# Kernel optimization log

Hardware: AMD Instinct MI355X
Metric: run time of the kernel (lower is better)

## Reference

```python
import jax, jax.numpy as jnp
import numpy as np

N, D = 16384, 128

def setup_inputs() -> dict:
    key = jax.random.key(0)
    k1, k2 = jax.random.split(key)
    x = jax.random.normal(k1, (N, D), dtype=jnp.float32)
    adj = jax.random.randint(k2, (N, N), 0, 2, dtype=jnp.int32)
    return {"x": x, "adj": adj}

def reference(x, adj):
    # out[i] = x[i] + sum_{j: adj[i,j]==1} x[j]  ==  (adj + I) @ x
    a = adj.astype(x.dtype)
    return x + jnp.matmul(a, x)  # [N, D]
```

## Files before the change

### kernel.cpp

```cpp
#include <hip/hip_runtime.h>
#include <hip/hip_bf16.h>

#define GN 16384
#define GD 128
#define KSPLIT 4
#define KBLK (GN / KSPLIT)
#define OUT_ELEMS (GN * GD)

typedef __attribute__((ext_vector_type(8))) short short8;
typedef __attribute__((ext_vector_type(4))) float floatx4;
typedef __attribute__((ext_vector_type(4))) int intx4;

static __device__ __forceinline__ unsigned short f32_to_bf16(float f) {
  unsigned u = __builtin_bit_cast(unsigned, f);
  unsigned r = u + 0x7FFFu + ((u >> 16) & 1u);
  return (unsigned short)(r >> 16);
}

__global__ __launch_bounds__(256) void prep_kernel(const float* __restrict__ x,
                                                   unsigned short* __restrict__ xT) {
  __shared__ unsigned short t[GD][66];
  const int tid = threadIdx.x;
  const int j0 = blockIdx.x * 64;
  for (int i = tid; i < 64 * GD; i += 256) {
    int j = i >> 7, d = i & (GD - 1);
    t[d][j] = f32_to_bf16(x[(size_t)(j0 + j) * GD + d]);
  }
  __syncthreads();
  for (int i = tid; i < GD * 32; i += 256) {
    int d = i >> 5, jp = i & 31;
    unsigned lo = t[d][2 * jp], hi = t[d][2 * jp + 1];
    *reinterpret_cast<unsigned*>(xT + (size_t)d * GN + j0 + 2 * jp) = lo | (hi << 16);
  }
}

__global__ __launch_bounds__(64, 2) void gemm_kernel(const int* __restrict__ adj,
                                                     const unsigned short* __restrict__ xT,
                                                     float* __restrict__ partials) {
  const int lane = threadIdx.x;
  const int q = lane >> 4;
  const int m = lane & 15;
  const int wid = blockIdx.x;
  const int rbase = (wid >> 2) * 32;
  const int ks = wid & 3;
  const int kbase = ks * KBLK;

  const int* a0 = adj + (size_t)(rbase + m) * GN + kbase + q * 8;
  const int* a1 = a0 + (size_t)16 * GN;
  const unsigned short* b0 = xT + (size_t)m * GN + kbase + q * 8;

  floatx4 acc[2][8];
#pragma unroll
  for (int t = 0; t < 2; ++t)
#pragma unroll
    for (int c = 0; c < 8; ++c) acc[t][c] = (floatx4){0.f, 0.f, 0.f, 0.f};

  intx4 r0 = __builtin_nontemporal_load((const intx4*)(a0));
  intx4 r1 = __builtin_nontemporal_load((const intx4*)(a0 + 4));
  intx4 r2 = __builtin_nontemporal_load((const intx4*)(a1));
  intx4 r3 = __builtin_nontemporal_load((const intx4*)(a1 + 4));
  short8 bf[8];
#pragma unroll
  for (int c = 0; c < 8; ++c)
    bf[c] = *(const short8*)(b0 + (size_t)c * 16 * GN);

  for (int k = 0; k < KBLK; k += 32) {
    const int kn = (k + 32) & (KBLK - 1);

    intx4 s0 = __builtin_nontemporal_load((const intx4*)(a0 + kn));
    intx4 s1 = __builtin_nontemporal_load((const intx4*)(a0 + kn + 4));
    intx4 s2 = __builtin_nontemporal_load((const intx4*)(a1 + kn));
    intx4 s3 = __builtin_nontemporal_load((const intx4*)(a1 + kn + 4));
    short8 nbf[8];
#pragma unroll
    for (int c = 0; c < 8; ++c)
      nbf[c] = *(const short8*)(b0 + (size_t)c * 16 * GN + kn);

    intx4 p0, p1;
    p0.x = (r0.x | (r0.y << 16)) * 0x3F80;
    p0.y = (r0.z | (r0.w << 16)) * 0x3F80;
    p0.z = (r1.x | (r1.y << 16)) * 0x3F80;
    p0.w = (r1.z | (r1.w << 16)) * 0x3F80;
    p1.x = (r2.x | (r2.y << 16)) * 0x3F80;
    p1.y = (r2.z | (r2.w << 16)) * 0x3F80;
    p1.z = (r3.x | (r3.y << 16)) * 0x3F80;
    p1.w = (r3.z | (r3.w << 16)) * 0x3F80;
    short8 af0 = __builtin_bit_cast(short8, p0);
    short8 af1 = __builtin_bit_cast(short8, p1);

#pragma unroll
    for (int c = 0; c < 8; ++c) {
      acc[0][c] = __builtin_amdgcn_mfma_f32_16x16x32_bf16(af0, bf[c], acc[0][c], 0, 0, 0);
      acc[1][c] = __builtin_amdgcn_mfma_f32_16x16x32_bf16(af1, bf[c], acc[1][c], 0, 0, 0);
    }

    r0 = s0; r1 = s1; r2 = s2; r3 = s3;
#pragma unroll
    for (int c = 0; c < 8; ++c) bf[c] = nbf[c];
  }

  float* pp = partials + (size_t)ks * OUT_ELEMS + (size_t)rbase * GD;
#pragma unroll
  for (int t = 0; t < 2; ++t)
#pragma unroll
    for (int c = 0; c < 8; ++c)
#pragma unroll
      for (int r = 0; r < 4; ++r) {
        int row = t * 16 + q * 4 + r;
        int col = c * 16 + m;
        pp[(size_t)row * GD + col] = acc[t][c][r];
      }
}

__global__ __launch_bounds__(256) void reduce_kernel(const float* __restrict__ x,
                                                     const float* __restrict__ partials,
                                                     float* __restrict__ out) {
  size_t i = ((size_t)blockIdx.x * 256 + threadIdx.x) * 4;
  floatx4 v = *(const floatx4*)(x + i);
  v += *(const floatx4*)(partials + 0 * (size_t)OUT_ELEMS + i);
  v += *(const floatx4*)(partials + 1 * (size_t)OUT_ELEMS + i);
  v += *(const floatx4*)(partials + 2 * (size_t)OUT_ELEMS + i);
  v += *(const floatx4*)(partials + 3 * (size_t)OUT_ELEMS + i);
  *(floatx4*)(out + i) = v;
}

extern "C" void kernel_launch(void* const* d_in, const int* in_sizes, int n_in,
                              void* d_out, int out_size, void* d_ws, size_t ws_size,
                              hipStream_t stream) {
  const float* x = (const float*)d_in[0];
  const int* adj = (const int*)d_in[1];
  float* out = (float*)d_out;
  unsigned short* xT = (unsigned short*)d_ws;
  float* partials = (float*)((char*)d_ws + (size_t)GN * GD * 2);

  prep_kernel<<<GN / 64, 256, 0, stream>>>(x, xT);
  gemm_kernel<<<(GN / 32) * KSPLIT, 64, 0, stream>>>(adj, xT, partials);
  reduce_kernel<<<OUT_ELEMS / 4 / 256, 256, 0, stream>>>(x, partials, out);
}
```

Before: 1.555 ms.

## Share B tiles across four waves via double-buffered LDS with direct global-to-LDS loads

The GEMM kernel moves from single-wave blocks that each read their own copy of the bf16 x^T tile from global memory to 256-thread blocks. In these, four waves share one B tile staged into a double-buffered, XOR-swizzled LDS buffer through global_load_lds. Each wave now covers 16 rows instead of 32, so it holds half the accumulators, which should allow higher occupancy. The intent is to cut redundant global/L2 traffic for B and leave more bandwidth for streaming the int32 adjacency matrix. The cost is a block-wide barrier on every k-step and LDS read overhead.

After: 1.373 ms. -11.8%, faster.

```diff
diff --git a/kernel.cpp b/kernel.cpp
--- a/kernel.cpp
+++ b/kernel.cpp
@@ -5,6 +5,9 @@
 #define GD 128
 #define KSPLIT 4
 #define KBLK (GN / KSPLIT)
+#define BK 64
+#define NPER (KBLK / BK)
+#define BUF_SHORTS (GD * BK)
 #define OUT_ELEMS (GN * GD)
 
 typedef __attribute__((ext_vector_type(8))) short short8;
@@ -34,82 +37,97 @@
   }
 }
 
-__global__ __launch_bounds__(64, 2) void gemm_kernel(const int* __restrict__ adj,
-                                                     const unsigned short* __restrict__ xT,
-                                                     float* __restrict__ partials) {
-  const int lane = threadIdx.x;
+__global__ __launch_bounds__(256, 4) void gemm_kernel(const int* __restrict__ adj,
+                                                      const unsigned short* __restrict__ xT,
+                                                      float* __restrict__ partials) {
+  __shared__ unsigned short bbuf[2][BUF_SHORTS];
+  const int tid = threadIdx.x;
+  const int wave = tid >> 6;
+  const int lane = tid & 63;
   const int q = lane >> 4;
   const int m = lane & 15;
-  const int wid = blockIdx.x;
-  const int rbase = (wid >> 2) * 32;
-  const int ks = wid & 3;
+  const int rbase = blockIdx.x * 64 + wave * 16;
+  const int ks = blockIdx.y;
   const int kbase = ks * KBLK;
 
+  const unsigned short* gptr[4];
+  unsigned short* lptr[4];
+#pragma unroll
+  for (int p = 0; p < 4; ++p) {
+    int s = tid + 256 * p;
+    int n = s >> 3;
+    int gsrc = (s & 7) ^ (n & 7);
+    gptr[p] = xT + (size_t)n * GN + kbase + gsrc * 8;
+    lptr[p] = &bbuf[0][0] + (size_t)s * 8;
+  }
+
+#define STAGE(bufsel, koff)                                                             \
+  do {                                                                                  \
+    _Pragma("unroll") for (int p = 0; p < 4; ++p) {                                     \
+      __builtin_amdgcn_global_load_lds(                                                 \
+          (const __attribute__((address_space(1))) unsigned int*)(gptr[p] + (koff)),    \
+          (__attribute__((address_space(3))) unsigned int*)(lptr[p] +                   \
+                                                           (bufsel) * BUF_SHORTS),      \
+          16, 0, 0);                                                                    \
+    }                                                                                   \
+  } while (0)
+
   const int* a0 = adj + (size_t)(rbase + m) * GN + kbase + q * 8;
-  const int* a1 = a0 + (size_t)16 * GN;
-  const unsigned short* b0 = xT + (size_t)m * GN + kbase + q * 8;
 
-  floatx4 acc[2][8];
+  floatx4 acc[8];
 #pragma unroll
-  for (int t = 0; t < 2; ++t)
-#pragma unroll
-    for (int c = 0; c < 8; ++c) acc[t][c] = (floatx4){0.f, 0.f, 0.f, 0.f};
+  for (int c = 0; c < 8; ++c) acc[c] = (floatx4){0.f, 0.f, 0.f, 0.f};
 
-  intx4 r0 = __builtin_nontemporal_load((const intx4*)(a0));
-  intx4 r1 = __builtin_nontemporal_load((const intx4*)(a0 + 4));
-  intx4 r2 = __builtin_nontemporal_load((const intx4*)(a1));
-  intx4 r3 = __builtin_nontemporal_load((const intx4*)(a1 + 4));
-  short8 bf[8];
-#pragma unroll
-  for (int c = 0; c < 8; ++c)
-    bf[c] = *(const short8*)(b0 + (size_t)c * 16 * GN);
+  STAGE(0, 0);
+  intx4 ca[4];
+  ca[0] = __builtin_nontemporal_load((const intx4*)(a0));
+  ca[1] = __builtin_nontemporal_load((const intx4*)(a0 + 4));
+  ca[2] = __builtin_nontemporal_load((const intx4*)(a0 + 32));
+  ca[3] = __builtin_nontemporal_load((const intx4*)(a0 + 36));
 
-  for (int k = 0; k < KBLK; k += 32) {
-    const int kn = (k + 32) & (KBLK - 1);
-
-    intx4 s0 = __builtin_nontemporal_load((const intx4*)(a0 + kn));
-    intx4 s1 = __builtin_nontemporal_load((const intx4*)(a0 + kn + 4));
-    intx4 s2 = __builtin_nontemporal_load((const intx4*)(a1 + kn));
-    intx4 s3 = __builtin_nontemporal_load((const intx4*)(a1 + kn + 4));
-    short8 nbf[8];
-#pragma unroll
-    for (int c = 0; c < 8; ++c)
-      nbf[c] = *(const short8*)(b0 + (size_t)c * 16 * GN + kn);
-
-    intx4 p0, p1;
-    p0.x = (r0.x | (r0.y << 16)) * 0x3F80;
-    p0.y = (r0.z | (r0.w << 16)) * 0x3F80;
-    p0.z = (r1.x | (r1.y << 16)) * 0x3F80;
-    p0.w = (r1.z | (r1.w << 16)) * 0x3F80;
-    p1.x = (r2.x | (r2.y << 16)) * 0x3F80;
-    p1.y = (r2.z | (r2.w << 16)) * 0x3F80;
-    p1.z = (r3.x | (r3.y << 16)) * 0x3F80;
-    p1.w = (r3.z | (r3.w << 16)) * 0x3F80;
-    short8 af0 = __builtin_bit_cast(short8, p0);
-    short8 af1 = __builtin_bit_cast(short8, p1);
+  int buf = 0;
+  for (int c = 0; c < NPER; ++c) {
+    __syncthreads();
+    const int nk = ((c + 1) & (NPER - 1)) * BK;
+    if (c + 1 < NPER) STAGE(buf ^ 1, nk);
+    intx4 na[4];
+    na[0] = __builtin_nontemporal_load((const intx4*)(a0 + nk));
+    na[1] = __builtin_nontemporal_load((const intx4*)(a0 + nk + 4));
+    na[2] = __builtin_nontemporal_load((const intx4*)(a0 + nk + 32));
+    na[3] = __builtin_nontemporal_load((const intx4*)(a0 + nk + 36));
 
 #pragma unroll
-    for (int c = 0; c < 8; ++c) {
-      acc[0][c] = __builtin_amdgcn_mfma_f32_16x16x32_bf16(af0, bf[c], acc[0][c], 0, 0, 0);
-      acc[1][c] = __builtin_amdgcn_mfma_f32_16x16x32_bf16(af1, bf[c], acc[1][c], 0, 0, 0);
+    for (int kk = 0; kk < 2; ++kk) {
+      short8 bf[8];
+      const unsigned short* bb = &bbuf[buf][0] + ((4 * kk + q) ^ (m & 7)) * 8;
+#pragma unroll
+      for (int cc = 0; cc < 8; ++cc)
+        bf[cc] = *(const short8*)(bb + (cc * 16 + m) * BK);
+
+      const intx4 r0 = ca[2 * kk], r1 = ca[2 * kk + 1];
+      intx4 pk;
+      pk.x = (r0.x | (r0.y << 16)) * 0x3F80;
+      pk.y = (r0.z | (r0.w << 16)) * 0x3F80;
+      pk.z = (r1.x | (r1.y << 16)) * 0x3F80;
+      pk.w = (r1.z | (r1.w << 16)) * 0x3F80;
+      const short8 af = __builtin_bit_cast(short8, pk);
+
+#pragma unroll
+      for (int cc = 0; cc < 8; ++cc)
+        acc[cc] = __builtin_amdgcn_mfma_f32_16x16x32_bf16(af, bf[cc], acc[cc], 0, 0, 0);
     }
 
-    r0 = s0; r1 = s1; r2 = s2; r3 = s3;
 #pragma unroll
-    for (int c = 0; c < 8; ++c) bf[c] = nbf[c];
+    for (int u = 0; u < 4; ++u) ca[u] = na[u];
+    buf ^= 1;
   }
 
   float* pp = partials + (size_t)ks * OUT_ELEMS + (size_t)rbase * GD;
 #pragma unroll
-  for (int t = 0; t < 2; ++t)
+  for (int cc = 0; cc < 8; ++cc)
 #pragma unroll
-    for (int c = 0; c < 8; ++c)
-#pragma unroll
-      for (int r = 0; r < 4; ++r) {
-        int row = t * 16 + q * 4 + r;
-        int col = c * 16 + m;
-        pp[(size_t)row * GD + col] = acc[t][c][r];
-      }
+    for (int r = 0; r < 4; ++r)
+      pp[(size_t)(q * 4 + r) * GD + cc * 16 + m] = acc[cc][r];
 }
 
 __global__ __launch_bounds__(256) void reduce_kernel(const float* __restrict__ x,
@@ -134,6 +152,6 @@
   float* partials = (float*)((char*)d_ws + (size_t)GN * GD * 2);
 
   prep_kernel<<<GN / 64, 256, 0, stream>>>(x, xT);
-  gemm_kernel<<<(GN / 32) * KSPLIT, 64, 0, stream>>>(adj, xT, partials);
+  gemm_kernel<<<dim3(GN / 64, KSPLIT), 256, 0, stream>>>(adj, xT, partials);
   reduce_kernel<<<OUT_ELEMS / 4 / 256, 256, 0, stream>>>(x, partials, out);
 }
```

## Pre-swizzle x into MFMA fragment layout and group four waves per block

Applied to the files above, without the earlier changes.

The prep kernel now writes x as bf16 in the exact per-lane MFMA B-fragment order, so each gemm lane loads its B operand with contiguous 16-byte reads instead of strided reads across rows of a transposed matrix. The gemm now runs four waves per 256-thread block covering 128 rows, and all four waves share the same K-split, so they read the same B tiles and can reuse them through cache. The adjacency streaming pattern is unchanged, and that stream is the dominant memory cost, so the benefit depends on how much B-load inefficiency actually mattered.

After: 1.466 ms. 1.06x faster.

```diff
diff --git a/kernel.cpp b/kernel.cpp
--- a/kernel.cpp
+++ b/kernel.cpp
@@ -5,6 +5,7 @@
 #define GD 128
 #define KSPLIT 4
 #define KBLK (GN / KSPLIT)
+#define NSTEP (KBLK / 32)
 #define OUT_ELEMS (GN * GD)
 
 typedef __attribute__((ext_vector_type(8))) short short8;
@@ -18,36 +19,44 @@
 }
 
 __global__ __launch_bounds__(256) void prep_kernel(const float* __restrict__ x,
-                                                   unsigned short* __restrict__ xT) {
-  __shared__ unsigned short t[GD][66];
+                                                   unsigned short* __restrict__ xT2) {
+  __shared__ unsigned short t[32][130];
+  const int g = blockIdx.x;
   const int tid = threadIdx.x;
-  const int j0 = blockIdx.x * 64;
-  for (int i = tid; i < 64 * GD; i += 256) {
-    int j = i >> 7, d = i & (GD - 1);
-    t[d][j] = f32_to_bf16(x[(size_t)(j0 + j) * GD + d]);
+  const float* xs = x + (size_t)g * 32 * GD;
+#pragma unroll
+  for (int i = 0; i < 16; ++i) {
+    int e = tid + 256 * i;
+    t[e >> 7][e & 127] = f32_to_bf16(xs[e]);
   }
   __syncthreads();
-  for (int i = tid; i < GD * 32; i += 256) {
-    int d = i >> 5, jp = i & 31;
-    unsigned lo = t[d][2 * jp], hi = t[d][2 * jp + 1];
-    *reinterpret_cast<unsigned*>(xT + (size_t)d * GN + j0 + 2 * jp) = lo | (hi << 16);
+  unsigned short* og = xT2 + (size_t)g * 4096;
+#pragma unroll
+  for (int h = 0; h < 2; ++h) {
+    int f = tid + 256 * h;
+    int cc = f >> 6, ln = f & 63, qq = ln >> 4, mm = ln & 15;
+    short8 v;
+#pragma unroll
+    for (int j = 0; j < 8; ++j) v[j] = (short)t[qq * 8 + j][cc * 16 + mm];
+    *(short8*)(og + (size_t)f * 8) = v;
   }
 }
 
-__global__ __launch_bounds__(64, 2) void gemm_kernel(const int* __restrict__ adj,
-                                                     const unsigned short* __restrict__ xT,
-                                                     float* __restrict__ partials) {
-  const int lane = threadIdx.x;
+__global__ __launch_bounds__(256, 2) void gemm_kernel(const int* __restrict__ adj,
+                                                      const unsigned short* __restrict__ xT2,
+                                                      float* __restrict__ partials) {
+  const int tid = threadIdx.x;
+  const int wave = tid >> 6;
+  const int lane = tid & 63;
   const int q = lane >> 4;
   const int m = lane & 15;
-  const int wid = blockIdx.x;
-  const int rbase = (wid >> 2) * 32;
-  const int ks = wid & 3;
+  const int rbase = blockIdx.x * 128 + wave * 32;
+  const int ks = blockIdx.y;
   const int kbase = ks * KBLK;
 
   const int* a0 = adj + (size_t)(rbase + m) * GN + kbase + q * 8;
   const int* a1 = a0 + (size_t)16 * GN;
-  const unsigned short* b0 = xT + (size_t)m * GN + kbase + q * 8;
+  const unsigned short* bp = xT2 + (size_t)(kbase / 32) * 4096 + (size_t)lane * 8;
 
   floatx4 acc[2][8];
 #pragma unroll
@@ -61,20 +70,19 @@
   intx4 r3 = __builtin_nontemporal_load((const intx4*)(a1 + 4));
   short8 bf[8];
 #pragma unroll
-  for (int c = 0; c < 8; ++c)
-    bf[c] = *(const short8*)(b0 + (size_t)c * 16 * GN);
+  for (int c = 0; c < 8; ++c) bf[c] = *(const short8*)(bp + c * 512);
 
-  for (int k = 0; k < KBLK; k += 32) {
-    const int kn = (k + 32) & (KBLK - 1);
+  for (int gl = 0; gl < NSTEP; ++gl) {
+    const int nk = ((gl + 1) & (NSTEP - 1)) * 32;
+    const unsigned short* bn = bp + ((gl + 1) & (NSTEP - 1)) * 4096;
 
-    intx4 s0 = __builtin_nontemporal_load((const intx4*)(a0 + kn));
-    intx4 s1 = __builtin_nontemporal_load((const intx4*)(a0 + kn + 4));
-    intx4 s2 = __builtin_nontemporal_load((const intx4*)(a1 + kn));
-    intx4 s3 = __builtin_nontemporal_load((const intx4*)(a1 + kn + 4));
+    intx4 s0 = __builtin_nontemporal_load((const intx4*)(a0 + nk));
+    intx4 s1 = __builtin_nontemporal_load((const intx4*)(a0 + nk + 4));
+    intx4 s2 = __builtin_nontemporal_load((const intx4*)(a1 + nk));
+    intx4 s3 = __builtin_nontemporal_load((const intx4*)(a1 + nk + 4));
     short8 nbf[8];
 #pragma unroll
-    for (int c = 0; c < 8; ++c)
-      nbf[c] = *(const short8*)(b0 + (size_t)c * 16 * GN + kn);
+    for (int c = 0; c < 8; ++c) nbf[c] = *(const short8*)(bn + c * 512);
 
     intx4 p0, p1;
     p0.x = (r0.x | (r0.y << 16)) * 0x3F80;
@@ -85,8 +93,8 @@
     p1.y = (r2.z | (r2.w << 16)) * 0x3F80;
     p1.z = (r3.x | (r3.y << 16)) * 0x3F80;
     p1.w = (r3.z | (r3.w << 16)) * 0x3F80;
-    short8 af0 = __builtin_bit_cast(short8, p0);
-    short8 af1 = __builtin_bit_cast(short8, p1);
+    const short8 af0 = __builtin_bit_cast(short8, p0);
+    const short8 af1 = __builtin_bit_cast(short8, p1);
 
 #pragma unroll
     for (int c = 0; c < 8; ++c) {
@@ -105,11 +113,8 @@
 #pragma unroll
     for (int c = 0; c < 8; ++c)
 #pragma unroll
-      for (int r = 0; r < 4; ++r) {
-        int row = t * 16 + q * 4 + r;
-        int col = c * 16 + m;
-        pp[(size_t)row * GD + col] = acc[t][c][r];
-      }
+      for (int r = 0; r < 4; ++r)
+        pp[(size_t)(t * 16 + q * 4 + r) * GD + c * 16 + m] = acc[t][c][r];
 }
 
 __global__ __launch_bounds__(256) void reduce_kernel(const float* __restrict__ x,
@@ -130,10 +135,10 @@
   const float* x = (const float*)d_in[0];
   const int* adj = (const int*)d_in[1];
   float* out = (float*)d_out;
-  unsigned short* xT = (unsigned short*)d_ws;
+  unsigned short* xT2 = (unsigned short*)d_ws;
   float* partials = (float*)((char*)d_ws + (size_t)GN * GD * 2);
 
-  prep_kernel<<<GN / 64, 256, 0, stream>>>(x, xT);
-  gemm_kernel<<<(GN / 32) * KSPLIT, 64, 0, stream>>>(adj, xT, partials);
+  prep_kernel<<<GN / 32, 256, 0, stream>>>(x, xT2);
+  gemm_kernel<<<dim3(GN / 128, KSPLIT), 256, 0, stream>>>(adj, xT2, partials);
   reduce_kernel<<<OUT_ELEMS / 4 / 256, 256, 0, stream>>>(x, partials, out);
 }
```
